# Kernel tuning notes

Hardware: AMD Instinct MI355X
Metric: run time of the kernel (lower is better)

Reference implementation:

```python
import jax, jax.numpy as jnp
import numpy as np

_COUNTS = [256, 192, 128, 64]


def _l2norm(x, axis=1):
    # F.normalize(p=2): x / max(||x||, eps)
    return x / jnp.maximum(jnp.linalg.norm(x, axis=axis, keepdims=True), 1e-12)


def _gcn(x, w1, b1, w2, b2, w3, b3):
    # stack of kernel-size-1 Conv1d == channel matmuls; x: [B, C, N]
    h = jax.nn.relu(jnp.einsum('oc,bcn->bon', w1, x) + b1[:, None])
    h = jax.nn.relu(jnp.einsum('oc,bcn->bon', w2, h) + b2[:, None])
    return jnp.einsum('oc,bcn->bon', w3, h) + b3[:, None]


def setup_inputs() -> dict:
    key = jax.random.key(0)
    ks = iter(jax.random.split(key, 64))
    feat_shapes = [(8, 256, 100, 100), (8, 512, 50, 50), (8, 1024, 25, 25), (8, 2048, 13, 13)]
    chans = [256, 512, 1024, 2048]
    C = 256
    d = {}
    for i, s in enumerate(feat_shapes):
        d[f'feat{i}'] = jax.random.normal(next(ks), s, jnp.float32)
    for i, (ci, ni) in enumerate(zip(chans, _COUNTS)):
        d[f'w_sem_{i}'] = jax.random.normal(next(ks), (ni, ci), jnp.float32) * 0.02
        d[f'w_emb_{i}'] = jax.random.normal(next(ks), (C, ci), jnp.float32) * 0.02
        d[f'w_q_{i}'] = jax.random.normal(next(ks), (C, ci), jnp.float32) * 0.02
        d[f'w_out_{i}'] = jax.random.normal(next(ks), (C, C), jnp.float32) * 0.02
        d[f'w_res_{i}'] = jax.random.normal(next(ks), (C, ci), jnp.float32) * 0.02
    d['gw1'] = jax.random.normal(next(ks), (4, 64, C), jnp.float32) * 0.05
    d['gb1'] = jnp.zeros((4, 64), jnp.float32)
    d['gw2'] = jax.random.normal(next(ks), (4, 64, 64), jnp.float32) * 0.05
    d['gb2'] = jnp.zeros((4, 64), jnp.float32)
    d['gw3'] = jax.random.normal(next(ks), (4, C, 64), jnp.float32) * 0.05
    d['gb3'] = jnp.zeros((4, C), jnp.float32)
    d['mw1'] = jax.random.normal(next(ks), (64, C), jnp.float32) * 0.05
    d['mb1'] = jnp.zeros((64,), jnp.float32)
    d['mw2'] = jax.random.normal(next(ks), (64, 64), jnp.float32) * 0.05
    d['mb2'] = jnp.zeros((64,), jnp.float32)
    d['mw3'] = jax.random.normal(next(ks), (C, 64), jnp.float32) * 0.05
    d['mb3'] = jnp.zeros((C,), jnp.float32)
    return d


def reference(feat0, feat1, feat2, feat3,
              w_sem_0, w_sem_1, w_sem_2, w_sem_3,
              w_emb_0, w_emb_1, w_emb_2, w_emb_3,
              w_q_0, w_q_1, w_q_2, w_q_3,
              w_out_0, w_out_1, w_out_2, w_out_3,
              w_res_0, w_res_1, w_res_2, w_res_3,
              gw1, gb1, gw2, gb2, gw3, gb3,
              mw1, mb1, mw2, mb2, mw3, mb3):
    feats = [feat0, feat1, feat2, feat3]
    w_sem = [w_sem_0, w_sem_1, w_sem_2, w_sem_3]
    w_emb = [w_emb_0, w_emb_1, w_emb_2, w_emb_3]
    w_q = [w_q_0, w_q_1, w_q_2, w_q_3]
    w_out = [w_out_0, w_out_1, w_out_2, w_out_3]
    w_res = [w_res_0, w_res_1, w_res_2, w_res_3]

    # ---- context collector ----
    contexts = []
    for i in range(4):
        f = feats[i]
        B, ci, H, W = f.shape
        hw = H * W
        sem = jnp.einsum('nc,bchw->bnhw', w_sem[i], f)                 # [B, ni, H, W]
        emb = jnp.einsum('oc,bchw->bohw', w_emb[i], f).reshape(B, -1, hw)  # [B, C, HW]
        fn = _l2norm(f, 1).reshape(B, ci, hw)
        en = _l2norm(sem, 1).reshape(B, -1, hw)
        # torch.einsum('bni,bci->bni') sums over c -> entities * sum_c(features)
        sim = en * fn.sum(axis=1, keepdims=True) * jnp.sqrt(jnp.float32(ci))
        attn = jax.nn.softmax(sim, axis=2)                              # softmax over HW
        contexts.append(jnp.einsum('bop,bnp->bon', emb, attn))          # [B, C, ni]

    # ---- graph reasoning ----
    refined = [_gcn(c, gw1[i], gb1[i], gw2[i], gb2[i], gw3[i], gb3[i]) + c
               for i, c in enumerate(contexts)]
    g = jnp.concatenate(refined, axis=2)                                # [B, C, 640]
    g = _gcn(g, mw1, mb1, mw2, mb2, mw3, mb3) + g

    # ---- context distributor ----
    outs = []
    ptr = 0
    for i in range(4):
        f = feats[i]
        B, ci, H, W = f.shape
        hw = H * W
        ni = _COUNTS[i]
        lc = g[:, :, ptr:ptr + ni]                                      # [B, C, ni]
        ptr += ni
        q = jnp.einsum('oc,bchw->bohw', w_q[i], f).reshape(B, -1, hw)   # [B, C, HW]
        scores = jnp.einsum('bop,bon->bpn', _l2norm(q, 1), _l2norm(lc, 1))  # [B, HW, ni]
        aw = jax.nn.softmax(scores, axis=2)                             # softmax over ni
        wc = jnp.einsum('bon,bpn->bop', lc, aw).reshape(B, -1, H, W)    # [B, C, H, W]
        out = jnp.einsum('oc,bchw->bohw', w_out[i], wc) + jnp.einsum('oc,bchw->bohw', w_res[i], f)
        outs.append(out)
    return tuple(outs)
```

## Files before the change

### kernel.cpp

```cpp
#include <hip/hip_runtime.h>
#include <math.h>


#define BB 8
#define CC 256
#define GG 640

typedef __attribute__((ext_vector_type(8))) short short8;
typedef __attribute__((ext_vector_type(4))) float f32x4;

__device__ __forceinline__ unsigned short f2bf(float f) {
    unsigned int u = __float_as_uint(f);
    u += 0x7fffu + ((u >> 16) & 1u);
    return (unsigned short)(u >> 16);
}
__device__ __forceinline__ float bf2f(unsigned short h) {
    return __uint_as_float(((unsigned int)h) << 16);
}
__device__ __forceinline__ float h2f(unsigned short h) {
    union { unsigned short u; _Float16 x; } cv; cv.u = h; return (float)cv.x;
}
__device__ __forceinline__ unsigned short f2h(float f) {
    union { unsigned short u; _Float16 x; } cv; cv.x = (_Float16)f; return cv.u;
}

__global__ __launch_bounds__(256) void mfmaGemm(
    const unsigned short* __restrict__ A, long sA, int lda,
    const unsigned short* __restrict__ B, long sB, int ldb,
    void* __restrict__ C, long sC, int ldc, long offC,
    int M, int N, int K, int kChunks, int kChunkLen, int mode)
{
    __shared__ __align__(16) unsigned short As[128 * 40];
    __shared__ __align__(16) unsigned short Bs[128 * 40];

    const int z = blockIdx.z;
    const int b = z / kChunks, chunk = z - b * kChunks;
    const int kbeg = chunk * kChunkLen;
    const int kend = min(K, kbeg + kChunkLen);

    const unsigned short* Ab = A + (long)b * sA;
    const unsigned short* Bb = B + (long)b * sB;
    const int m0 = blockIdx.y * 128, n0 = blockIdx.x * 128;

    const int tid = threadIdx.x;
    const int wave = tid >> 6, lane = tid & 63;
    const int wm = (wave & 1) * 64, wn = (wave >> 1) * 64;
    const int lm = lane & 15, kq = lane >> 4;
    const int lrow = tid >> 2;
    const int q4 = tid & 3;

    const bool alignedA = ((lda & 7) == 0) && ((((size_t)Ab) & 15) == 0);
    const bool alignedB = ((ldb & 7) == 0) && ((((size_t)Bb) & 15) == 0);

    f32x4 acc[4][4];
    #pragma unroll
    for (int i = 0; i < 4; ++i)
        #pragma unroll
        for (int j = 0; j < 4; ++j) acc[i][j] = (f32x4){0.f, 0.f, 0.f, 0.f};

    uint4 pa[2], pb[2];
    auto fetch = [&](int k0) {
        int kg = k0 + q4 * 8;
        int krem = kend - kg;
        #pragma unroll
        for (int l = 0; l < 2; ++l) {
            int row = l * 64 + lrow;
            uint4 va = make_uint4(0u, 0u, 0u, 0u);
            int gm = m0 + row;
            if (gm < M && krem > 0) {
                const unsigned short* src = Ab + (long)gm * lda + kg;
                if (krem >= 8 && alignedA) {
                    va = *(const uint4*)src;
                } else {
                    __align__(16) unsigned short tmp[8] = {0,0,0,0,0,0,0,0};
                    int c = krem < 8 ? krem : 8;
                    for (int j = 0; j < c; ++j) tmp[j] = src[j];
                    va = *(const uint4*)tmp;
                }
            }
            pa[l] = va;
            uint4 vb = make_uint4(0u, 0u, 0u, 0u);
            int gn = n0 + row;
            if (gn < N && krem > 0) {
                const unsigned short* src = Bb + (long)gn * ldb + kg;
                if (krem >= 8 && alignedB) {
                    vb = *(const uint4*)src;
                } else {
                    __align__(16) unsigned short tmp[8] = {0,0,0,0,0,0,0,0};
                    int c = krem < 8 ? krem : 8;
                    for (int j = 0; j < c; ++j) tmp[j] = src[j];
                    vb = *(const uint4*)tmp;
                }
            }
            pb[l] = vb;
        }
    };

    fetch(kbeg);
    for (int k0 = kbeg; k0 < kend; k0 += 32) {
        __syncthreads();
        *(uint4*)&As[lrow * 40 + q4 * 8]        = pa[0];
        *(uint4*)&As[(64 + lrow) * 40 + q4 * 8] = pa[1];
        *(uint4*)&Bs[lrow * 40 + q4 * 8]        = pb[0];
        *(uint4*)&Bs[(64 + lrow) * 40 + q4 * 8] = pb[1];
        __syncthreads();
        if (k0 + 32 < kend) fetch(k0 + 32);

        short8 af[4], bfr[4];
        #pragma unroll
        for (int mt = 0; mt < 4; ++mt)
            af[mt] = *(const short8*)&As[(wm + mt * 16 + lm) * 40 + kq * 8];
        #pragma unroll
        for (int nt = 0; nt < 4; ++nt)
            bfr[nt] = *(const short8*)&Bs[(wn + nt * 16 + lm) * 40 + kq * 8];
        #pragma unroll
        for (int mt = 0; mt < 4; ++mt)
            #pragma unroll
            for (int nt = 0; nt < 4; ++nt)
                acc[mt][nt] = __builtin_amdgcn_mfma_f32_16x16x32_bf16(
                    af[mt], bfr[nt], acc[mt][nt], 0, 0, 0);
    }

    const long cbase = (long)b * sC + offC;
    #pragma unroll
    for (int mt = 0; mt < 4; ++mt) {
        #pragma unroll
        for (int nt = 0; nt < 4; ++nt) {
            int n_g = n0 + wn + nt * 16 + lm;
            if (n_g >= N) continue;
            #pragma unroll
            for (int r = 0; r < 4; ++r) {
                int m_g = m0 + wm + mt * 16 + kq * 4 + r;
                if (m_g >= M) continue;
                float v = acc[mt][nt][r];
                long ci_ = cbase + (long)m_g * ldc + n_g;
                if (mode == 0)      ((float*)C)[ci_] = v;
                else if (mode == 1) ((float*)C)[ci_] += v;
                else if (mode == 2) atomicAdd(&((float*)C)[ci_], v);
                else if (mode == 3) ((unsigned short*)C)[ci_] = f2h(v);
                else                ((unsigned short*)C)[ci_] = f2bf(v);
            }
        }
    }
}

__global__ __launch_bounds__(256) void gemmA(
    const float* __restrict__ W, long sW,
    const float* __restrict__ X, long sX, int ldx, long offX,
    float* __restrict__ Cd, long sC, int ldc, long offC,
    const float* __restrict__ bias,
    const float* __restrict__ res, long sR, int ldr, long offR,
    int O, int K, int P, int relu, int accum,
    int lvlFuse, long wStride, int bStride)
{
    __shared__ float Ws[16][64];
    __shared__ float Xs[16][64];
    const int tid = threadIdx.x;
    const int tx = tid & 15;
    const int ty = tid >> 4;
    const int b  = blockIdx.z;
    const int o0 = blockIdx.y * 64;
    const int p0 = blockIdx.x * 64;

    const float* Wp = W;
    const float* bp = bias;
    if (lvlFuse) {
        int lvl = p0 >= 576 ? 3 : p0 >= 448 ? 2 : p0 >= 256 ? 1 : 0;
        Wp += (long)lvl * wStride;
        if (bias) bp += (long)lvl * bStride;
    }
    const float* Wb = Wp + (long)b * sW;
    const float* Xb = X + (long)b * sX + offX;

    float acc[4][4] = {};

    const int wo = tid >> 2;
    const int wk = (tid & 3) * 4;
    const int xp = tid & 63;
    const int xq = tid >> 6;

    for (int k0 = 0; k0 < K; k0 += 16) {
        #pragma unroll
        for (int u = 0; u < 4; ++u) {
            int kk = wk + u;
            float v = 0.f;
            if (o0 + wo < O && k0 + kk < K) v = Wb[(long)(o0 + wo) * K + k0 + kk];
            Ws[kk][wo] = v;
        }
        #pragma unroll
        for (int u = 0; u < 4; ++u) {
            int kk = xq * 4 + u;
            float v = 0.f;
            if (p0 + xp < P && k0 + kk < K) v = Xb[(long)(k0 + kk) * ldx + (p0 + xp)];
            Xs[kk][xp] = v;
        }
        __syncthreads();
        #pragma unroll
        for (int kk = 0; kk < 16; ++kk) {
            float4 wv = *(const float4*)&Ws[kk][ty * 4];
            float4 xv = *(const float4*)&Xs[kk][tx * 4];
            float wa[4] = {wv.x, wv.y, wv.z, wv.w};
            float xa[4] = {xv.x, xv.y, xv.z, xv.w};
            #pragma unroll
            for (int i = 0; i < 4; ++i)
                #pragma unroll
                for (int j = 0; j < 4; ++j)
                    acc[i][j] += wa[i] * xa[j];
        }
        __syncthreads();
    }

    #pragma unroll
    for (int i = 0; i < 4; ++i) {
        int o = o0 + ty * 4 + i;
        if (o >= O) continue;
        #pragma unroll
        for (int j = 0; j < 4; ++j) {
            int p = p0 + tx * 4 + j;
            if (p >= P) continue;
            float v = acc[i][j];
            if (bias) v += bp[o];
            if (relu) v = fmaxf(v, 0.f);
            if (res)  v += res[(long)b * sR + offR + (long)o * ldr + p];
            long ci_ = (long)b * sC + offC + (long)o * ldc + p;
            if (accum) Cd[ci_] += v; else Cd[ci_] = v;
        }
    }
}

__global__ __launch_bounds__(256) void transCvtF(
    const float* __restrict__ src, long sS, int R, int Cc,
    unsigned short* __restrict__ dst, long sD,
    const float* __restrict__ scale, long sScale)
{
    __shared__ float tile[32][33];
    int b = blockIdx.z;
    int r0 = blockIdx.y * 32, c0 = blockIdx.x * 32;
    const float* sb = src + (long)b * sS;
    unsigned short* db = dst + (long)b * sD;
    int tr = threadIdx.x >> 5, tc = threadIdx.x & 31;
    #pragma unroll
    for (int it = 0; it < 4; ++it) {
        int r = r0 + tr + it * 8, c = c0 + tc;
        tile[tr + it * 8][tc] = (r < R && c < Cc) ? sb[(long)r * Cc + c] : 0.f;
    }
    __syncthreads();
    #pragma unroll
    for (int it = 0; it < 4; ++it) {
        int c = c0 + tr + it * 8;
        int r = r0 + tc;
        if (c < Cc && r < R) {
            float v = tile[tc][tr + it * 8];
            if (scale) v *= scale[(long)b * sScale + c];
            db[(long)c * R + r] = f2bf(v);
        }
    }
}

__global__ __launch_bounds__(256) void transCvtH(
    const unsigned short* __restrict__ src, long sS, int R, int Cc,
    unsigned short* __restrict__ dst, long sD,
    const float* __restrict__ scale, long sScale)
{
    __shared__ float tile[32][33];
    int b = blockIdx.z;
    int r0 = blockIdx.y * 32, c0 = blockIdx.x * 32;
    const unsigned short* sb = src + (long)b * sS;
    unsigned short* db = dst + (long)b * sD;
    int tr = threadIdx.x >> 5, tc = threadIdx.x & 31;
    #pragma unroll
    for (int it = 0; it < 4; ++it) {
        int r = r0 + tr + it * 8, c = c0 + tc;
        tile[tr + it * 8][tc] = (r < R && c < Cc) ? h2f(sb[(long)r * Cc + c]) : 0.f;
    }
    __syncthreads();
    #pragma unroll
    for (int it = 0; it < 4; ++it) {
        int c = c0 + tr + it * 8;
        int r = r0 + tc;
        if (c < Cc && r < R) {
            float v = tile[tc][tr + it * 8];
            if (scale) v *= scale[(long)b * sScale + c];
            db[(long)c * R + r] = f2bf(v);
        }
    }
}

__global__ __launch_bounds__(256) void posStatsT(
    const unsigned short* __restrict__ featT, float* __restrict__ fscale,
    int ci, int hw, float sq)
{
    int b = blockIdx.y, p = blockIdx.x;
    const unsigned short* row = featT + ((long)b * hw + p) * ci;
    float s = 0.f, ss = 0.f;
    for (int c = threadIdx.x; c < ci; c += 256) {
        float v = bf2f(row[c]); s += v; ss += v * v;
    }
    __shared__ float rs[256], rss[256];
    int tid = threadIdx.x;
    rs[tid] = s; rss[tid] = ss; __syncthreads();
    for (int st = 128; st > 0; st >>= 1) {
        if (tid < st) { rs[tid] += rs[tid + st]; rss[tid] += rss[tid + st]; }
        __syncthreads();
    }
    if (tid == 0)
        fscale[(long)b * hw + p] = rs[0] / fmaxf(sqrtf(rss[0]), 1e-12f) * sq;
}

__global__ void enScale(const unsigned short* __restrict__ sem, float* __restrict__ fscale,
                        int ni, int hw)
{
    int b = blockIdx.y;
    int p = blockIdx.x * 256 + threadIdx.x;
    if (p >= hw) return;
    const unsigned short* sb = sem + (long)b * ni * hw + p;
    float ss = 0.f;
    for (int n = 0; n < ni; ++n) { float v = h2f(sb[(long)n * hw]); ss += v * v; }
    fscale[(long)b * hw + p] = fscale[(long)b * hw + p] / fmaxf(sqrtf(ss), 1e-12f);
}

__global__ __launch_bounds__(256) void softmaxHW(
    unsigned short* buf, const float* __restrict__ scale, int ni, int hw)
{
    int b = blockIdx.y, n = blockIdx.x;
    unsigned short* row = buf + ((long)b * ni + n) * hw;
    const float* sc = scale + (long)b * hw;
    __shared__ float red[256];
    int tid = threadIdx.x;

    float m = -1e30f;
    for (int p = tid; p < hw; p += 256) m = fmaxf(m, h2f(row[p]) * sc[p]);
    red[tid] = m; __syncthreads();
    for (int s = 128; s > 0; s >>= 1) {
        if (tid < s) red[tid] = fmaxf(red[tid], red[tid + s]);
        __syncthreads();
    }
    m = red[0]; __syncthreads();

    float sum = 0.f;
    for (int p = tid; p < hw; p += 256) sum += __expf(h2f(row[p]) * sc[p] - m);
    red[tid] = sum; __syncthreads();
    for (int s = 128; s > 0; s >>= 1) {
        if (tid < s) red[tid] += red[tid + s];
        __syncthreads();
    }
    float inv = 1.0f / red[0];

    for (int p = tid; p < hw; p += 256) {
        float v = __expf(h2f(row[p]) * sc[p] - m) * inv;
        row[p] = f2bf(v);
    }
}

__global__ void softmaxN(unsigned short* buf, int hw, int ni)
{
    int b = blockIdx.y;
    int wav = threadIdx.x >> 6, lane = threadIdx.x & 63;
    int p = blockIdx.x * 4 + wav;
    if (p >= hw) return;
    unsigned short* row = buf + ((long)b * hw + p) * ni;
    float m = -1e30f;
    for (int n = lane; n < ni; n += 64) m = fmaxf(m, h2f(row[n]));
    for (int off = 32; off > 0; off >>= 1) m = fmaxf(m, __shfl_xor(m, off));
    float s = 0.f;
    for (int n = lane; n < ni; n += 64) s += __expf(h2f(row[n]) - m);
    for (int off = 32; off > 0; off >>= 1) s += __shfl_xor(s, off);
    float inv = 1.f / s;
    for (int n = lane; n < ni; n += 64) {
        float v = __expf(h2f(row[n]) - m) * inv;
        row[n] = f2bf(v);
    }
}

__global__ void lcRnorm(const float* __restrict__ g2, float* __restrict__ lcr)
{
    int b = blockIdx.y;
    int col = blockIdx.x * 256 + threadIdx.x;
    if (col >= GG) return;
    const float* gb = g2 + (long)b * CC * GG + col;
    float ss = 0.f;
    for (int o = 0; o < CC; ++o) { float v = gb[o * GG]; ss += v * v; }
    lcr[b * GG + col] = 1.f / fmaxf(sqrtf(ss), 1e-12f);
}

__global__ void buildLc(const float* __restrict__ g2, const float* __restrict__ lcr,
                        unsigned short* __restrict__ lcnT, unsigned short* __restrict__ lcB,
                        int ni, int ptr)
{
    long t = (long)blockIdx.x * 256 + threadIdx.x;
    if (t >= (long)BB * ni * CC) return;
    int o = (int)(t & (CC - 1));
    long r = t >> 8;
    int n = (int)(r % ni);
    int b = (int)(r / ni);
    float raw = g2[(long)b * CC * GG + (long)o * GG + ptr + n];
    lcnT[t] = f2bf(raw * lcr[b * GG + ptr + n]);
    lcB[((long)b * CC + o) * ni + n] = f2bf(raw);
}

__global__ void qNormCol(const unsigned short* __restrict__ q, float* __restrict__ scl, int hw)
{
    int b = blockIdx.y;
    int p = blockIdx.x * 256 + threadIdx.x;
    if (p >= hw) return;
    const unsigned short* qb = q + (long)b * CC * hw + p;
    float ss = 0.f;
    for (int o = 0; o < CC; ++o) { float v = h2f(qb[(long)o * hw]); ss += v * v; }
    scl[(long)b * hw + p] = 1.f / fmaxf(sqrtf(ss), 1e-12f);
}

struct CvtJob { const float* src; long off; int n; int pad; };
struct CvtJobs { CvtJob j[20]; };
__global__ void cvtAllK(CvtJobs jobs, unsigned short* __restrict__ dst)
{
    const CvtJob J = jobs.j[blockIdx.y];
    int t = blockIdx.x * 256 + threadIdx.x;
    if (t < J.n) dst[J.off + t] = f2bf(J.src[t]);
}

__global__ void cvtOut(const float* __restrict__ src, unsigned short* __restrict__ dst,
                       int n, int toF16)
{
    int i = blockIdx.x * 256 + threadIdx.x;
    if (i >= n) return;
    float v = src[i];
    dst[i] = toF16 ? f2h(v) : f2bf(v);
}

extern "C" void kernel_launch(void* const* d_in, const int* in_sizes, int n_in,
                              void* d_out, int out_size, void* d_ws, size_t ws_size,
                              hipStream_t stream)
{
    (void)n_in; (void)out_size; (void)ws_size;
    static const int  CI[4]  = {256, 512, 1024, 2048};
    static const int  NI[4]  = {256, 192, 128, 64};
    static const int  HWs[4] = {10000, 2500, 625, 169};
    static const int  PTR[4] = {0, 256, 448, 576};
    static const long OUTOFF[4] = {0, 20480000L, 25600000L, 26880000L};

    const float* feat[4];
    for (int i = 0; i < 4; ++i) feat[i] = (const float*)d_in[i];

    const float *w_sem[4], *w_emb[4], *w_q[4], *w_out[4], *w_res[4];
    bool grouped = (in_sizes[5] == 192 * 512);
    for (int i = 0; i < 4; ++i) {
        if (grouped) {
            w_sem[i] = (const float*)d_in[4 + i];
            w_emb[i] = (const float*)d_in[8 + i];
            w_q[i]   = (const float*)d_in[12 + i];
            w_out[i] = (const float*)d_in[16 + i];
            w_res[i] = (const float*)d_in[20 + i];
        } else {
            int base = 4 + 5 * i;
            w_sem[i] = (const float*)d_in[base + 0];
            w_emb[i] = (const float*)d_in[base + 1];
            w_q[i]   = (const float*)d_in[base + 2];
            w_out[i] = (const float*)d_in[base + 3];
            w_res[i] = (const float*)d_in[base + 4];
        }
    }
    const float* gw1 = (const float*)d_in[24];
    const float* gb1 = (const float*)d_in[25];
    const float* gw2 = (const float*)d_in[26];
    const float* gb2 = (const float*)d_in[27];
    const float* gw3 = (const float*)d_in[28];
    const float* gb3 = (const float*)d_in[29];
    const float* mw1 = (const float*)d_in[30];
    const float* mb1 = (const float*)d_in[31];
    const float* mw2 = (const float*)d_in[32];
    const float* mb2 = (const float*)d_in[33];
    const float* mw3 = (const float*)d_in[34];
    const float* mb3 = (const float*)d_in[35];

    char* wp = (char*)d_ws;
    auto carve = [&](size_t bytes) { char* r = wp; wp += (bytes + 255) & ~(size_t)255; return r; };
    unsigned short* R1 = (unsigned short*)carve(40960000);
    unsigned short* R2 = (unsigned short*)carve(40960000);
    unsigned short* R3 = (unsigned short*)carve(40960000);
    float* ctxg = (float*)carve(5242880);
    float* gbuf = (float*)carve(5242880);
    float* g2   = (float*)carve(5242880);
    float* h1   = (float*)carve(1310720);
    float* h2   = (float*)carve(1310720);
    unsigned short* lcnT = (unsigned short*)carve(1048576);
    unsigned short* lcB  = (unsigned short*)carve(1048576);
    float* lcr  = (float*)carve(20480);
    float* scl  = (float*)carve(320000);
    float* SK   = (float*)carve(5120000);
    unsigned short* wbuf = (unsigned short*)carve(7275520);

    float* outp = (float*)d_out;

    CvtJobs jobs;
    unsigned short *wsemB[4], *wembB[4], *wqB[4], *woutB[4], *wresB[4];
    long woff = 0; int maxn = 0, jx = 0;
    auto addJob = [&](const float* s, int n, unsigned short** outp_) {
        jobs.j[jx].src = s; jobs.j[jx].off = woff; jobs.j[jx].n = n; jobs.j[jx].pad = 0;
        *outp_ = wbuf + woff;
        woff += (n + 7) & ~7;
        if (n > maxn) maxn = n;
        ++jx;
    };
    for (int i = 0; i < 4; ++i) {
        addJob(w_sem[i], NI[i] * CI[i], &wsemB[i]);
        addJob(w_emb[i], CC * CI[i],    &wembB[i]);
        addJob(w_q[i],   CC * CI[i],    &wqB[i]);
        addJob(w_out[i], CC * CC,       &woutB[i]);
        addJob(w_res[i], CC * CI[i],    &wresB[i]);
    }
    cvtAllK<<<dim3((maxn + 255) / 256, 20), 256, 0, stream>>>(jobs, wbuf);

    auto mg = [&](const unsigned short* A, long sA, int lda,
                  const unsigned short* Bp, long sB, int ldb,
                  void* Cp, long sC, int ldc, long offC,
                  int M, int N, int K, int mode, int kc) {
        if (kc < 1) kc = 1;
        int kLen = ((K + kc - 1) / kc + 31) & ~31;
        int kcc = (K + kLen - 1) / kLen;
        dim3 g((N + 127) / 128, (M + 127) / 128, BB * kcc);
        mfmaGemm<<<g, 256, 0, stream>>>(A, sA, lda, Bp, sB, ldb,
                                        Cp, sC, ldc, offC, M, N, K, kcc, kLen, mode);
    };
    auto projTo = [&](const unsigned short* Wbf, int K, const unsigned short* Xt, long sXt,
                      unsigned short* dst, int M, int N, int fmode) {
        int blocks = ((M + 127) / 128) * ((N + 127) / 128) * BB;
        if (blocks >= 256 || K < 512) {
            mg(Wbf, 0, K, Xt, sXt, K, dst, (long)M * N, N, 0, M, N, K, fmode, 1);
        } else {
            int kc = (256 + blocks - 1) / blocks;
            hipMemsetAsync(SK, 0, (size_t)BB * M * N * 4, stream);
            mg(Wbf, 0, K, Xt, sXt, K, SK, (long)M * N, N, 0, M, N, K, 2, kc);
            long tot = (long)BB * M * N;
            cvtOut<<<dim3((unsigned)((tot + 255) / 256)), 256, 0, stream>>>(
                SK, dst, (int)tot, fmode == 3 ? 1 : 0);
        }
    };

    hipMemsetAsync(ctxg, 0, (size_t)BB * CC * GG * 4, stream);

    for (int i = 0; i < 4; ++i) {
        int ci = CI[i], ni = NI[i], hw = HWs[i];
        transCvtF<<<dim3((hw + 31) / 32, (ci + 31) / 32, BB), 256, 0, stream>>>(
            feat[i], (long)ci * hw, ci, hw, R1, (long)hw * ci, nullptr, 0);
        posStatsT<<<dim3(hw, BB), 256, 0, stream>>>(R1, scl, ci, hw, sqrtf((float)ci));
        projTo(wsemB[i], ci, R1, (long)hw * ci, R2, ni, hw, 3);
        enScale<<<dim3((hw + 255) / 256, BB), 256, 0, stream>>>(R2, scl, ni, hw);
        projTo(wembB[i], ci, R1, (long)hw * ci, R3, CC, hw, 4);
        softmaxHW<<<dim3(ni, BB), 256, 0, stream>>>(R2, scl, ni, hw);
        {
            int blocks = ((CC + 127) / 128) * ((ni + 127) / 128) * BB;
            int kc = (blocks < 256 && hw >= 512) ? (256 + blocks - 1) / blocks : 1;
            mg(R3, (long)CC * hw, hw, R2, (long)ni * hw, hw,
               ctxg, (long)CC * GG, GG, PTR[i], CC, ni, hw, 2, kc);
        }
    }

    {
        dim3 gl(GG / 64, 1, BB);
        gemmA<<<gl, 256, 0, stream>>>(gw1, 0, ctxg, (long)CC * GG, GG, 0,
                                      h1, (long)64 * GG, GG, 0, gb1,
                                      nullptr, 0, 0, 0, 64, CC, GG, 1, 0,
                                      1, (long)64 * CC, 64);
        gemmA<<<gl, 256, 0, stream>>>(gw2, 0, h1, (long)64 * GG, GG, 0,
                                      h2, (long)64 * GG, GG, 0, gb2,
                                      nullptr, 0, 0, 0, 64, 64, GG, 1, 0,
                                      1, (long)64 * 64, 64);
        dim3 gl2(GG / 64, CC / 64, BB);
        gemmA<<<gl2, 256, 0, stream>>>(gw3, 0, h2, (long)64 * GG, GG, 0,
                                       gbuf, (long)CC * GG, GG, 0, gb3,
                                       ctxg, (long)CC * GG, GG, 0, CC, 64, GG, 0, 0,
                                       1, (long)CC * 64, CC);
    }
    {
        dim3 gl(GG / 64, 1, BB);
        gemmA<<<gl, 256, 0, stream>>>(mw1, 0, gbuf, (long)CC * GG, GG, 0,
                                      h1, (long)64 * GG, GG, 0, mb1,
                                      nullptr, 0, 0, 0, 64, CC, GG, 1, 0, 0, 0, 0);
        gemmA<<<gl, 256, 0, stream>>>(mw2, 0, h1, (long)64 * GG, GG, 0,
                                      h2, (long)64 * GG, GG, 0, mb2,
                                      nullptr, 0, 0, 0, 64, 64, GG, 1, 0, 0, 0, 0);
        dim3 gl2(GG / 64, CC / 64, BB);
        gemmA<<<gl2, 256, 0, stream>>>(mw3, 0, h2, (long)64 * GG, GG, 0,
                                       g2, (long)CC * GG, GG, 0, mb3,
                                       gbuf, (long)CC * GG, GG, 0, CC, 64, GG, 0, 0, 0, 0, 0);
    }

    lcRnorm<<<dim3(3, BB), 256, 0, stream>>>(g2, lcr);

    for (int i = 0; i < 4; ++i) {
        int ci = CI[i], ni = NI[i], hw = HWs[i];
        long tot = (long)BB * ni * CC;
        buildLc<<<dim3((unsigned)((tot + 255) / 256)), 256, 0, stream>>>(
            g2, lcr, lcnT, lcB, ni, PTR[i]);
        transCvtF<<<dim3((hw + 31) / 32, (ci + 31) / 32, BB), 256, 0, stream>>>(
            feat[i], (long)ci * hw, ci, hw, R1, (long)hw * ci, nullptr, 0);
        projTo(wqB[i], ci, R1, (long)hw * ci, R2, CC, hw, 3);
        qNormCol<<<dim3((hw + 255) / 256, BB), 256, 0, stream>>>(R2, scl, hw);
        transCvtH<<<dim3((hw + 31) / 32, (CC + 31) / 32, BB), 256, 0, stream>>>(
            R2, (long)CC * hw, CC, hw, R3, (long)hw * CC, scl, hw);
        mg(R3, (long)hw * CC, CC, lcnT, (long)ni * CC, CC,
           R2, (long)hw * ni, ni, 0, hw, ni, CC, 3, 1);
        softmaxN<<<dim3((hw + 3) / 4, BB), 256, 0, stream>>>(R2, hw, ni);
        mg(R2, (long)hw * ni, ni, lcB, (long)CC * ni, ni,
           R3, (long)hw * CC, CC, 0, hw, CC, ni, 4, 1);
        {
            int blocks = ((CC + 127) / 128) * ((hw + 127) / 128) * BB;
            if (blocks >= 256 || ci < 512) {
                mg(wresB[i], 0, ci, R1, (long)hw * ci, ci,
                   outp, (long)CC * hw, hw, OUTOFF[i], CC, hw, ci, 0, 1);
            } else {
                int kc = (256 + blocks - 1) / blocks;
                hipMemsetAsync(outp + OUTOFF[i], 0, (size_t)BB * CC * hw * 4, stream);
                mg(wresB[i], 0, ci, R1, (long)hw * ci, ci,
                   outp, (long)CC * hw, hw, OUTOFF[i], CC, hw, ci, 2, kc);
            }
        }
        mg(woutB[i], 0, CC, R3, (long)hw * CC, CC,
           outp, (long)CC * hw, hw, OUTOFF[i], CC, hw, CC, 1, 1);
    }
}
```

Measured before the change: 2.205 ms.

## Double-buffer GEMM with direct global-to-LDS loads, XCD swizzle, fused projections, persistent feats

The bf16 MFMA GEMM now stages tiles straight into double-buffered LDS with global_load_lds, which removes one barrier per K step and the register round trip. A 1D grid is remapped for XCD locality. Stacked weights fuse the semantic and embedding projections, and the query and residual projections, into one GEMM with split outputs for the two large levels. Transposed bf16 features persist in the workspace so the second transpose pass is skipped. The cost is more workspace, padding-free LDS rows that may cause bank conflicts, and stacked weights that rely on wsem/wemb and wq/wres being adjacent in the buffer.

```diff
diff --git a/kernel.cpp b/kernel.cpp
--- a/kernel.cpp
+++ b/kernel.cpp
@@ -24,33 +24,49 @@
     union { unsigned short u; _Float16 x; } cv; cv.x = (_Float16)f; return cv.u;
 }
 
+__device__ __forceinline__ void glds16(const unsigned short* g, unsigned short* l) {
+    __builtin_amdgcn_global_load_lds(
+        (const __attribute__((address_space(1))) void*)g,
+        (__attribute__((address_space(3))) void*)l, 16, 0, 0);
+}
+
 __global__ __launch_bounds__(256) void mfmaGemm(
     const unsigned short* __restrict__ A, long sA, int lda,
     const unsigned short* __restrict__ B, long sB, int ldb,
     void* __restrict__ C, long sC, int ldc, long offC,
-    int M, int N, int K, int kChunks, int kChunkLen, int mode)
-{
-    __shared__ __align__(16) unsigned short As[128 * 40];
-    __shared__ __align__(16) unsigned short Bs[128 * 40];
-
-    const int z = blockIdx.z;
+    int M, int N, int K, int kChunks, int kChunkLen, int mode,
+    int gxn, int gym,
+    void* __restrict__ C2, long sC2, int ldc2, long offC2, int M1, int mode2)
+{
+    __shared__ __align__(16) unsigned short As[2][128 * 32];
+    __shared__ __align__(16) unsigned short Bs[2][128 * 32];
+
+    const int nb = (int)gridDim.x;
+    int orig = (int)blockIdx.x;
+    int xcd = orig & 7, idx = orig >> 3;
+    int q8 = nb >> 3, r8 = nb & 7;
+    int wg = (xcd < r8) ? (xcd * (q8 + 1) + idx)
+                        : (r8 * (q8 + 1) + (xcd - r8) * q8 + idx);
+    int mb, nbk, z;
+    if (N >= M) { mb = wg % gym; int t = wg / gym; nbk = t % gxn; z = t / gxn; }
+    else        { nbk = wg % gxn; int t = wg / gxn; mb = t % gym; z = t / gym; }
+
     const int b = z / kChunks, chunk = z - b * kChunks;
     const int kbeg = chunk * kChunkLen;
     const int kend = min(K, kbeg + kChunkLen);
+    const int m0 = mb * 128, n0 = nbk * 128;
 
     const unsigned short* Ab = A + (long)b * sA;
     const unsigned short* Bb = B + (long)b * sB;
-    const int m0 = blockIdx.y * 128, n0 = blockIdx.x * 128;
 
     const int tid = threadIdx.x;
+    const int row = tid >> 2, seg = tid & 3;
     const int wave = tid >> 6, lane = tid & 63;
     const int wm = (wave & 1) * 64, wn = (wave >> 1) * 64;
     const int lm = lane & 15, kq = lane >> 4;
-    const int lrow = tid >> 2;
-    const int q4 = tid & 3;
-
-    const bool alignedA = ((lda & 7) == 0) && ((((size_t)Ab) & 15) == 0);
-    const bool alignedB = ((ldb & 7) == 0) && ((((size_t)Bb) & 15) == 0);
+
+    const bool okA = ((lda & 7) == 0) && ((((size_t)Ab) & 15) == 0);
+    const bool okB = ((ldb & 7) == 0) && ((((size_t)Bb) & 15) == 0);
 
     f32x4 acc[4][4];
     #pragma unroll
@@ -58,70 +74,68 @@
         #pragma unroll
         for (int j = 0; j < 4; ++j) acc[i][j] = (f32x4){0.f, 0.f, 0.f, 0.f};
 
-    uint4 pa[2], pb[2];
-    auto fetch = [&](int k0) {
-        int kg = k0 + q4 * 8;
-        int krem = kend - kg;
+    auto stageF = [&](const unsigned short* Pb, int ld, int o0,
+                      unsigned short* LS, int kg) {
         #pragma unroll
         for (int l = 0; l < 2; ++l) {
-            int row = l * 64 + lrow;
-            uint4 va = make_uint4(0u, 0u, 0u, 0u);
-            int gm = m0 + row;
-            if (gm < M && krem > 0) {
-                const unsigned short* src = Ab + (long)gm * lda + kg;
-                if (krem >= 8 && alignedA) {
-                    va = *(const uint4*)src;
+            const unsigned short* src = Pb + (long)(o0 + l * 64 + row) * ld + kg + seg * 8;
+            glds16(src, &LS[(l * 64 + row) * 32 + seg * 8]);
+        }
+    };
+    auto stageS = [&](const unsigned short* Pb, int ld, int lim, int o0,
+                      unsigned short* LS, int kg) {
+        int kgg = kg + seg * 8;
+        int krem = kend - kgg;
+        #pragma unroll
+        for (int l = 0; l < 2; ++l) {
+            int g = o0 + l * 64 + row;
+            uint4 v = make_uint4(0u, 0u, 0u, 0u);
+            if (g < lim && krem > 0) {
+                const unsigned short* src = Pb + (long)g * ld + kgg;
+                if (krem >= 8 && ((((size_t)src) & 15) == 0)) {
+                    v = *(const uint4*)src;
                 } else {
                     __align__(16) unsigned short tmp[8] = {0,0,0,0,0,0,0,0};
                     int c = krem < 8 ? krem : 8;
                     for (int j = 0; j < c; ++j) tmp[j] = src[j];
-                    va = *(const uint4*)tmp;
+                    v = *(const uint4*)tmp;
                 }
             }
-            pa[l] = va;
-            uint4 vb = make_uint4(0u, 0u, 0u, 0u);
-            int gn = n0 + row;
-            if (gn < N && krem > 0) {
-                const unsigned short* src = Bb + (long)gn * ldb + kg;
-                if (krem >= 8 && alignedB) {
-                    vb = *(const uint4*)src;
-                } else {
-                    __align__(16) unsigned short tmp[8] = {0,0,0,0,0,0,0,0};
-                    int c = krem < 8 ? krem : 8;
-                    for (int j = 0; j < c; ++j) tmp[j] = src[j];
-                    vb = *(const uint4*)tmp;
-                }
-            }
-            pb[l] = vb;
+            *(uint4*)&LS[(l * 64 + row) * 32 + seg * 8] = v;
         }
     };
-
-    fetch(kbeg);
+    auto stage = [&](int kg, int buf) {
+        bool full = (kg + 32 <= kend);
+        if (okA && full) stageF(Ab, lda, m0, As[buf], kg);
+        else             stageS(Ab, lda, M, m0, As[buf], kg);
+        if (okB && full) stageF(Bb, ldb, n0, Bs[buf], kg);
+        else             stageS(Bb, ldb, N, n0, Bs[buf], kg);
+    };
+
+    stage(kbeg, 0);
+    int cur = 0;
     for (int k0 = kbeg; k0 < kend; k0 += 32) {
         __syncthreads();
-        *(uint4*)&As[lrow * 40 + q4 * 8]        = pa[0];
-        *(uint4*)&As[(64 + lrow) * 40 + q4 * 8] = pa[1];
-        *(uint4*)&Bs[lrow * 40 + q4 * 8]        = pb[0];
-        *(uint4*)&Bs[(64 + lrow) * 40 + q4 * 8] = pb[1];
-        __syncthreads();
-        if (k0 + 32 < kend) fetch(k0 + 32);
+        if (k0 + 32 < kend) stage(k0 + 32, cur ^ 1);
 
         short8 af[4], bfr[4];
         #pragma unroll
         for (int mt = 0; mt < 4; ++mt)
-            af[mt] = *(const short8*)&As[(wm + mt * 16 + lm) * 40 + kq * 8];
+            af[mt] = *(const short8*)&As[cur][(wm + mt * 16 + lm) * 32 + kq * 8];
         #pragma unroll
         for (int nt = 0; nt < 4; ++nt)
-            bfr[nt] = *(const short8*)&Bs[(wn + nt * 16 + lm) * 40 + kq * 8];
+            bfr[nt] = *(const short8*)&Bs[cur][(wn + nt * 16 + lm) * 32 + kq * 8];
         #pragma unroll
         for (int mt = 0; mt < 4; ++mt)
             #pragma unroll
             for (int nt = 0; nt < 4; ++nt)
                 acc[mt][nt] = __builtin_amdgcn_mfma_f32_16x16x32_bf16(
                     af[mt], bfr[nt], acc[mt][nt], 0, 0, 0);
-    }
-
-    const long cbase = (long)b * sC + offC;
+        cur ^= 1;
+    }
+
+    const long cb1 = (long)b * sC + offC;
+    const long cb2 = (long)b * sC2 + offC2;
     #pragma unroll
     for (int mt = 0; mt < 4; ++mt) {
         #pragma unroll
@@ -133,12 +147,14 @@
                 int m_g = m0 + wm + mt * 16 + kq * 4 + r;
                 if (m_g >= M) continue;
                 float v = acc[mt][nt][r];
-                long ci_ = cbase + (long)m_g * ldc + n_g;
-                if (mode == 0)      ((float*)C)[ci_] = v;
-                else if (mode == 1) ((float*)C)[ci_] += v;
-                else if (mode == 2) atomicAdd(&((float*)C)[ci_], v);
-                else if (mode == 3) ((unsigned short*)C)[ci_] = f2h(v);
-                else                ((unsigned short*)C)[ci_] = f2bf(v);
+                void* Cp; int md; long cix;
+                if (m_g < M1) { Cp = C;  md = mode;  cix = cb1 + (long)m_g * ldc + n_g; }
+                else          { Cp = C2; md = mode2; cix = cb2 + (long)(m_g - M1) * ldc2 + n_g; }
+                if (md == 0)      ((float*)Cp)[cix] = v;
+                else if (md == 1) ((float*)Cp)[cix] += v;
+                else if (md == 2) atomicAdd(&((float*)Cp)[cix], v);
+                else if (md == 3) ((unsigned short*)Cp)[cix] = f2h(v);
+                else              ((unsigned short*)Cp)[cix] = f2bf(v);
             }
         }
     }
@@ -431,7 +447,7 @@
                               void* d_out, int out_size, void* d_ws, size_t ws_size,
                               hipStream_t stream)
 {
-    (void)n_in; (void)out_size; (void)ws_size;
+    (void)n_in; (void)out_size;
     static const int  CI[4]  = {256, 512, 1024, 2048};
     static const int  NI[4]  = {256, 192, 128, 64};
     static const int  HWs[4] = {10000, 2500, 625, 169};
@@ -489,6 +505,25 @@
     float* SK   = (float*)carve(5120000);
     unsigned short* wbuf = (unsigned short*)carve(7275520);
 
+    unsigned short* featP[4];
+    featP[0] = R1;
+    {
+        size_t f1 = 2UL * BB * 2500 * 512;
+        size_t f2 = 2UL * BB * 625 * 1024;
+        size_t f3 = 2UL * BB * 169 * 2048;
+        size_t used = (size_t)(wp - (char*)d_ws);
+        bool persist = (used + f1 + f2 + f3 + (1u << 20) + 4096) <= ws_size;
+        if (persist) {
+            featP[1] = (unsigned short*)carve(f1);
+            featP[2] = (unsigned short*)carve(f2);
+            featP[3] = (unsigned short*)carve(f3);
+            carve(1u << 20);
+        } else {
+            featP[1] = featP[2] = featP[3] = R1;
+        }
+    }
+    bool persist = (featP[1] != R1);
+
     float* outp = (float*)d_out;
 
     CvtJobs jobs;
@@ -505,21 +540,31 @@
         addJob(w_sem[i], NI[i] * CI[i], &wsemB[i]);
         addJob(w_emb[i], CC * CI[i],    &wembB[i]);
         addJob(w_q[i],   CC * CI[i],    &wqB[i]);
+        addJob(w_res[i], CC * CI[i],    &wresB[i]);
         addJob(w_out[i], CC * CC,       &woutB[i]);
-        addJob(w_res[i], CC * CI[i],    &wresB[i]);
     }
     cvtAllK<<<dim3((maxn + 255) / 256, 20), 256, 0, stream>>>(jobs, wbuf);
 
+    auto mgSeg = [&](const unsigned short* A, long sA, int lda,
+                     const unsigned short* Bp, long sB, int ldb,
+                     void* Cp, long sC, int ldc, long offC,
+                     int M, int N, int K, int mode, int kc,
+                     void* C2, long sC2, int ldc2, long offC2, int M1, int mode2) {
+        if (kc < 1) kc = 1;
+        int kLen = ((K + kc - 1) / kc + 31) & ~31;
+        int kcc = (K + kLen - 1) / kLen;
+        int gxn = (N + 127) / 128, gym = (M + 127) / 128;
+        dim3 g((unsigned)(gxn * gym * BB * kcc));
+        mfmaGemm<<<g, 256, 0, stream>>>(A, sA, lda, Bp, sB, ldb,
+                                        Cp, sC, ldc, offC, M, N, K, kcc, kLen, mode,
+                                        gxn, gym, C2, sC2, ldc2, offC2, M1, mode2);
+    };
     auto mg = [&](const unsigned short* A, long sA, int lda,
                   const unsigned short* Bp, long sB, int ldb,
                   void* Cp, long sC, int ldc, long offC,
                   int M, int N, int K, int mode, int kc) {
-        if (kc < 1) kc = 1;
-        int kLen = ((K + kc - 1) / kc + 31) & ~31;
-        int kcc = (K + kLen - 1) / kLen;
-        dim3 g((N + 127) / 128, (M + 127) / 128, BB * kcc);
-        mfmaGemm<<<g, 256, 0, stream>>>(A, sA, lda, Bp, sB, ldb,
-                                        Cp, sC, ldc, offC, M, N, K, kcc, kLen, mode);
+        mgSeg(A, sA, lda, Bp, sB, ldb, Cp, sC, ldc, offC, M, N, K, mode, kc,
+              nullptr, 0, 1, 0, M, 0);
     };
     auto projTo = [&](const unsigned short* Wbf, int K, const unsigned short* Xt, long sXt,
                       unsigned short* dst, int M, int N, int fmode) {
@@ -540,12 +585,20 @@
 
     for (int i = 0; i < 4; ++i) {
         int ci = CI[i], ni = NI[i], hw = HWs[i];
+        unsigned short* fT = featP[i];
         transCvtF<<<dim3((hw + 31) / 32, (ci + 31) / 32, BB), 256, 0, stream>>>(
-            feat[i], (long)ci * hw, ci, hw, R1, (long)hw * ci, nullptr, 0);
-        posStatsT<<<dim3(hw, BB), 256, 0, stream>>>(R1, scl, ci, hw, sqrtf((float)ci));
-        projTo(wsemB[i], ci, R1, (long)hw * ci, R2, ni, hw, 3);
+            feat[i], (long)ci * hw, ci, hw, fT, (long)hw * ci, nullptr, 0);
+        posStatsT<<<dim3(hw, BB), 256, 0, stream>>>(fT, scl, ci, hw, sqrtf((float)ci));
+        if (i < 2) {
+            mgSeg(wsemB[i], 0, ci, fT, (long)hw * ci, ci,
+                  R2, (long)ni * hw, hw, 0,
+                  ni + CC, hw, ci, 3, 1,
+                  R3, (long)CC * hw, hw, 0, ni, 4);
+        } else {
+            projTo(wsemB[i], ci, fT, (long)hw * ci, R2, ni, hw, 3);
+            projTo(wembB[i], ci, fT, (long)hw * ci, R3, CC, hw, 4);
+        }
         enScale<<<dim3((hw + 255) / 256, BB), 256, 0, stream>>>(R2, scl, ni, hw);
-        projTo(wembB[i], ci, R1, (long)hw * ci, R3, CC, hw, 4);
         softmaxHW<<<dim3(ni, BB), 256, 0, stream>>>(R2, scl, ni, hw);
         {
             int blocks = ((CC + 127) / 128) * ((ni + 127) / 128) * BB;
@@ -592,9 +645,18 @@
         long tot = (long)BB * ni * CC;
         buildLc<<<dim3((unsigned)((tot + 255) / 256)), 256, 0, stream>>>(
             g2, lcr, lcnT, lcB, ni, PTR[i]);
-        transCvtF<<<dim3((hw + 31) / 32, (ci + 31) / 32, BB), 256, 0, stream>>>(
-            feat[i], (long)ci * hw, ci, hw, R1, (long)hw * ci, nullptr, 0);
-        projTo(wqB[i], ci, R1, (long)hw * ci, R2, CC, hw, 3);
+        unsigned short* fT = featP[i];
+        if (!persist)
+            transCvtF<<<dim3((hw + 31) / 32, (ci + 31) / 32, BB), 256, 0, stream>>>(
+                feat[i], (long)ci * hw, ci, hw, fT, (long)hw * ci, nullptr, 0);
+        if (i < 2) {
+            mgSeg(wqB[i], 0, ci, fT, (long)hw * ci, ci,
+                  R2, (long)CC * hw, hw, 0,
+                  2 * CC, hw, ci, 3, 1,
+                  outp, (long)CC * hw, hw, OUTOFF[i], CC, 0);
+        } else {
+            projTo(wqB[i], ci, fT, (long)hw * ci, R2, CC, hw, 3);
+        }
         qNormCol<<<dim3((hw + 255) / 256, BB), 256, 0, stream>>>(R2, scl, hw);
         transCvtH<<<dim3((hw + 31) / 32, (CC + 31) / 32, BB), 256, 0, stream>>>(
             R2, (long)CC * hw, CC, hw, R3, (long)hw * CC, scl, hw);
@@ -603,15 +665,15 @@
         softmaxN<<<dim3((hw + 3) / 4, BB), 256, 0, stream>>>(R2, hw, ni);
         mg(R2, (long)hw * ni, ni, lcB, (long)CC * ni, ni,
            R3, (long)hw * CC, CC, 0, hw, CC, ni, 4, 1);
-        {
+        if (i >= 2) {
             int blocks = ((CC + 127) / 128) * ((hw + 127) / 128) * BB;
             if (blocks >= 256 || ci < 512) {
-                mg(wresB[i], 0, ci, R1, (long)hw * ci, ci,
+                mg(wresB[i], 0, ci, fT, (long)hw * ci, ci,
                    outp, (long)CC * hw, hw, OUTOFF[i], CC, hw, ci, 0, 1);
             } else {
                 int kc = (256 + blocks - 1) / blocks;
                 hipMemsetAsync(outp + OUTOFF[i], 0, (size_t)BB * CC * hw * 4, stream);
-                mg(wresB[i], 0, ci, R1, (long)hw * ci, ci,
+                mg(wresB[i], 0, ci, fT, (long)hw * ci, ci,
                    outp, (long)CC * hw, hw, OUTOFF[i], CC, hw, ci, 2, kc);
             }
         }
```

Result: faster. 2.127 ms (-3.5%).
